# Kernel tuning notes

Measured on AMD Instinct MI355X. Metric: run time of the kernel, lower is better.

The kernel has to match this reference:

```python
import jax, jax.numpy as jnp
import numpy as np

HIDDEN = 256
HEADS = 8
HEAD_DIM = HIDDEN // HEADS
SCALE = HEAD_DIM ** -0.5
N = 4096
NUM_GRAPHS = 16
LN_EPS = 1e-5


def setup_inputs() -> dict:
    key = jax.random.key(0)
    ks = jax.random.split(key, 8)
    x = jax.random.normal(ks[0], (N, HIDDEN), dtype=jnp.float32)
    batch = jnp.sort(jax.random.randint(ks[1], (N,), 0, NUM_GRAPHS, dtype=jnp.int64))
    # Xavier-uniform linear weights, stored as [in, out] (y = x @ W + b)
    lim = float(np.sqrt(6.0 / (HIDDEN + HIDDEN)))
    def W(k):
        return jax.random.uniform(k, (HIDDEN, HIDDEN), jnp.float32, -lim, lim)
    return {
        "x": x,
        "batch": batch,
        "Wq": W(ks[2]), "bq": jnp.zeros((HIDDEN,), jnp.float32),
        "Wk": W(ks[3]), "bk": jnp.zeros((HIDDEN,), jnp.float32),
        "Wv": W(ks[4]), "bv": jnp.zeros((HIDDEN,), jnp.float32),
        "Wo": W(ks[5]), "bo": jnp.zeros((HIDDEN,), jnp.float32),
        "gamma": jnp.ones((HIDDEN,), jnp.float32),
        "beta": jnp.zeros((HIDDEN,), jnp.float32),
    }


def _layer_norm(x, gamma, beta):
    mu = jnp.mean(x, axis=-1, keepdims=True)
    var = jnp.mean(jnp.square(x - mu), axis=-1, keepdims=True)
    return (x - mu) * jax.lax.rsqrt(var + LN_EPS) * gamma + beta


def reference(x, batch, Wq, bq, Wk, bk, Wv, bv, Wo, bo, gamma, beta):
    residual = x
    h = _layer_norm(x, gamma, beta)
    n = h.shape[0]
    q = (h @ Wq + bq).reshape(n, HEADS, HEAD_DIM)
    k = (h @ Wk + bk).reshape(n, HEADS, HEAD_DIM)
    v = (h @ Wv + bv).reshape(n, HEADS, HEAD_DIM)
    # dense scores masked to block-diagonal (same-graph) structure
    scores = jnp.einsum('ihd,jhd->ihj', q, k) * SCALE  # [N, H, N]
    same_graph = (batch[None, :] == batch[:, None])[:, None, :]  # [N, 1, N]
    scores = jnp.where(same_graph, scores, -jnp.inf)
    attn = jax.nn.softmax(scores, axis=-1)
    attn = jnp.nan_to_num(attn, nan=0.0)
    out = jnp.einsum('ihj,jhd->ihd', attn, v).reshape(n, HIDDEN)
    out = out @ Wo + bo
    return residual + out
```

## Files before the change

### kernel.cpp

```cpp
#include <hip/hip_runtime.h>

#define NNODES 4096
#define HID 256
#define NG 16
#define NH 8
#define HD 32
#define LN_EPS 1e-5f
#define QSCALE (0.17677669529663687f * 1.4426950408889634f)
#define HLS 264

typedef unsigned short u16;
typedef unsigned int u32;
typedef __bf16 bf16x8 __attribute__((ext_vector_type(8)));
typedef float f32x4 __attribute__((ext_vector_type(4)));

__device__ __forceinline__ u16 f2bf(float f){
  union { float f; u32 i; } c; c.f = f;
  u32 x = c.i;
  return (u16)((x + 0x7fffu + ((x >> 16) & 1u)) >> 16);
}

__global__ __launch_bounds__(256) void lnqkv_kernel(
    const float* __restrict__ x, const float* __restrict__ gamma,
    const float* __restrict__ beta,
    const float* __restrict__ Wq, const float* __restrict__ Wk,
    const float* __restrict__ Wv,
    const float* __restrict__ bq, const float* __restrict__ bk,
    const float* __restrict__ bv,
    u16* __restrict__ qb, u16* __restrict__ kb, u16* __restrict__ vb){
  __shared__ u16 hl[64][HLS];
  int bid = blockIdx.x;
  int which = blockIdx.y;
  int wave = threadIdx.x >> 6, lane = threadIdx.x & 63;
  int m0 = (bid >> 2) * 64;
  int nb = (bid & 3) * 64 + wave * 16;
  const float* W    = (which == 0) ? Wq : (which == 1) ? Wk : Wv;
  const float* bias = (which == 0) ? bq : (which == 1) ? bk : bv;
  u16* out          = (which == 0) ? qb : (which == 1) ? kb : vb;

  int rsub = lane >> 4;
  int c16  = lane & 15;
  float4 g0 = *(const float4*)(gamma + c16 * 16 + 0);
  float4 g1 = *(const float4*)(gamma + c16 * 16 + 4);
  float4 g2 = *(const float4*)(gamma + c16 * 16 + 8);
  float4 g3 = *(const float4*)(gamma + c16 * 16 + 12);
  float4 t0 = *(const float4*)(beta + c16 * 16 + 0);
  float4 t1 = *(const float4*)(beta + c16 * 16 + 4);
  float4 t2 = *(const float4*)(beta + c16 * 16 + 8);
  float4 t3 = *(const float4*)(beta + c16 * 16 + 12);
  float ga[16] = {g0.x,g0.y,g0.z,g0.w, g1.x,g1.y,g1.z,g1.w,
                  g2.x,g2.y,g2.z,g2.w, g3.x,g3.y,g3.z,g3.w};
  float bt[16] = {t0.x,t0.y,t0.z,t0.w, t1.x,t1.y,t1.z,t1.w,
                  t2.x,t2.y,t2.z,t2.w, t3.x,t3.y,t3.z,t3.w};
  #pragma unroll
  for (int b = 0; b < 4; b++){
    int rloc = wave * 16 + b * 4 + rsub;
    const float* xr = x + (size_t)(m0 + rloc) * HID + c16 * 16;
    float4 v0 = *(const float4*)(xr + 0);
    float4 v1 = *(const float4*)(xr + 4);
    float4 v2 = *(const float4*)(xr + 8);
    float4 v3 = *(const float4*)(xr + 12);
    float e[16] = {v0.x,v0.y,v0.z,v0.w, v1.x,v1.y,v1.z,v1.w,
                   v2.x,v2.y,v2.z,v2.w, v3.x,v3.y,v3.z,v3.w};
    float s = 0.f;
    #pragma unroll
    for (int i = 0; i < 16; i++) s += e[i];
    s += __shfl_xor(s, 1); s += __shfl_xor(s, 2);
    s += __shfl_xor(s, 4); s += __shfl_xor(s, 8);
    float mu = s * (1.0f / HID);
    float vv = 0.f;
    #pragma unroll
    for (int i = 0; i < 16; i++){ e[i] -= mu; vv += e[i] * e[i]; }
    vv += __shfl_xor(vv, 1); vv += __shfl_xor(vv, 2);
    vv += __shfl_xor(vv, 4); vv += __shfl_xor(vv, 8);
    float rs = rsqrtf(vv * (1.0f / HID) + LN_EPS);
    u32 pk[8];
    #pragma unroll
    for (int i = 0; i < 8; i++){
      float o0 = e[2*i]     * rs * ga[2*i]     + bt[2*i];
      float o1 = e[2*i + 1] * rs * ga[2*i + 1] + bt[2*i + 1];
      pk[i] = (u32)f2bf(o0) | ((u32)f2bf(o1) << 16);
    }
    *(uint4*)&hl[rloc][c16 * 16]     = make_uint4(pk[0], pk[1], pk[2], pk[3]);
    *(uint4*)&hl[rloc][c16 * 16 + 8] = make_uint4(pk[4], pk[5], pk[6], pk[7]);
  }
  __syncthreads();

  int lr = lane & 15, lq = lane >> 4;
  f32x4 acc[4] = {};
  const float* wbase = W + nb + lr;
  #pragma unroll
  for (int k0 = 0; k0 < HID; k0 += 32){
    union { bf16x8 v; u16 e[8]; } bf;
    const float* wp = wbase + (size_t)(k0 + lq * 8) * HID;
    #pragma unroll
    for (int j = 0; j < 8; j++) bf.e[j] = f2bf(wp[(size_t)j * HID]);
    #pragma unroll
    for (int t = 0; t < 4; t++){
      bf16x8 a = *(const bf16x8*)&hl[t * 16 + lr][k0 + lq * 8];
      acc[t] = __builtin_amdgcn_mfma_f32_16x16x32_bf16(a, bf.v, acc[t], 0, 0, 0);
    }
  }
  int col = nb + lr;
  float bb = bias[col];
  #pragma unroll
  for (int t = 0; t < 4; t++){
    #pragma unroll
    for (int r = 0; r < 4; r++){
      int row = m0 + 16 * t + lq * 4 + r;
      out[(size_t)row * HID + col] = f2bf(acc[t][r] + bb);
    }
  }
}

__global__ __launch_bounds__(512, 4) void attn_kernel(const u16* __restrict__ q,
    const u16* __restrict__ k, const u16* __restrict__ v,
    const int* __restrict__ batch, int bstride, u16* __restrict__ out){
  __shared__ float mg[4][10][64];
  __shared__ int s_se[2];
  int gh = blockIdx.y;
  int g = gh >> 3, hd = gh & 7;
  int wave = threadIdx.x >> 6, lane = threadIdx.x & 63;
  if (wave < 2){
    int target = g + wave;
    int p = batch[(size_t)(lane * 64) * bstride];
    int c = __popcll(__ballot(p < target));
    int lo = 0;
    if (c > 0){
      int base = (c - 1) * 64 + 1;
      int idx = base + lane;
      int val = (idx < NNODES) ? batch[(size_t)idx * bstride] : 0x7fffffff;
      lo = base + __popcll(__ballot(val < target));
    }
    if (lane == 0) s_se[wave] = lo;
  }
  __syncthreads();
  int start = s_se[0], end = s_se[1];
  int len = end - start;
  if (len <= 0) return;
  int ntj = (len + 15) >> 4;
  int lq = lane >> 4, lr = lane & 15;
  int tl = wave & 3;
  int jh = wave >> 2;
  int nouter = (ntj + 15) >> 4;
  for (int it = 0; it < nouter; it++){
    int tq = it * 16 + blockIdx.x * 4 + tl;
    bool active = tq < ntj;
    int q0 = tq << 4;
    float m = -3.0e38f, l = 0.f;
    f32x4 o0 = {0.f,0.f,0.f,0.f}, o1 = {0.f,0.f,0.f,0.f};
    if (active){
      bf16x8 qf = *(const bf16x8*)&q[(size_t)(start + q0 + lr) * HID + hd * HD + lq * 8];
      int half = (ntj + 1) >> 1;
      int jt0 = jh ? half : 0;
      int jt1 = jh ? ntj : half;
      for (int jt = jt0; jt < jt1; jt++){
        int j0 = jt << 4;
        int krow = start + j0 + lr;
        if (krow > NNODES - 1) krow = NNODES - 1;
        bf16x8 kf = *(const bf16x8*)&k[(size_t)krow * HID + hd * HD + lq * 8];
        u16 va[4], vc[4];
        #pragma unroll
        for (int i = 0; i < 4; i++){
          int vrow = start + j0 + lq * 4 + i;
          if (vrow > NNODES - 1) vrow = NNODES - 1;
          const u16* vp = &v[(size_t)vrow * HID + hd * HD + lr];
          va[i] = vp[0];
          vc[i] = vp[16];
        }
        f32x4 st = __builtin_amdgcn_mfma_f32_16x16x32_bf16(kf, qf,
                     (f32x4){0.f,0.f,0.f,0.f}, 0, 0, 0);
        int jb = j0 + lq * 4;
        float s0 = (jb + 0 < len) ? st[0] * QSCALE : -3.0e38f;
        float s1 = (jb + 1 < len) ? st[1] * QSCALE : -3.0e38f;
        float s2 = (jb + 2 < len) ? st[2] * QSCALE : -3.0e38f;
        float s3 = (jb + 3 < len) ? st[3] * QSCALE : -3.0e38f;
        float tm = fmaxf(fmaxf(s0, s1), fmaxf(s2, s3));
        tm = fmaxf(tm, __shfl_xor(tm, 16));
        tm = fmaxf(tm, __shfl_xor(tm, 32));
        float mn = fmaxf(m, tm);
        float alpha = exp2f(m - mn);
        float p0 = exp2f(s0 - mn), p1 = exp2f(s1 - mn);
        float p2 = exp2f(s2 - mn), p3 = exp2f(s3 - mn);
        float ps = (p0 + p1) + (p2 + p3);
        ps += __shfl_xor(ps, 16);
        ps += __shfl_xor(ps, 32);
        l = l * alpha + ps;
        m = mn;
        union { bf16x8 v8; u32 w[4]; } pf, vf0, vf1;
        pf.w[0] = (u32)f2bf(p0) | ((u32)f2bf(p1) << 16);
        pf.w[1] = (u32)f2bf(p2) | ((u32)f2bf(p3) << 16);
        pf.w[2] = 0; pf.w[3] = 0;
        vf0.w[0] = (u32)va[0] | ((u32)va[1] << 16);
        vf0.w[1] = (u32)va[2] | ((u32)va[3] << 16);
        vf0.w[2] = 0; vf0.w[3] = 0;
        vf1.w[0] = (u32)vc[0] | ((u32)vc[1] << 16);
        vf1.w[1] = (u32)vc[2] | ((u32)vc[3] << 16);
        vf1.w[2] = 0; vf1.w[3] = 0;
        o0 = o0 * alpha;
        o1 = o1 * alpha;
        o0 = __builtin_amdgcn_mfma_f32_16x16x32_bf16(vf0.v8, pf.v8, o0, 0, 0, 0);
        o1 = __builtin_amdgcn_mfma_f32_16x16x32_bf16(vf1.v8, pf.v8, o1, 0, 0, 0);
      }
    }
    if (jh == 1){
      mg[tl][0][lane] = o0[0]; mg[tl][1][lane] = o0[1];
      mg[tl][2][lane] = o0[2]; mg[tl][3][lane] = o0[3];
      mg[tl][4][lane] = o1[0]; mg[tl][5][lane] = o1[1];
      mg[tl][6][lane] = o1[2]; mg[tl][7][lane] = o1[3];
      mg[tl][8][lane] = m;     mg[tl][9][lane] = l;
    }
    __syncthreads();
    if (jh == 0 && active && q0 + lr < len){
      float m2 = mg[tl][8][lane], l2 = mg[tl][9][lane];
      float mn = fmaxf(m, m2);
      float a  = exp2f(m - mn);
      float a2 = exp2f(m2 - mn);
      float lt = l * a + l2 * a2;
      float rl = 1.0f / lt;
      float r0 = (o0[0]*a + mg[tl][0][lane]*a2) * rl;
      float r1 = (o0[1]*a + mg[tl][1][lane]*a2) * rl;
      float r2 = (o0[2]*a + mg[tl][2][lane]*a2) * rl;
      float r3 = (o0[3]*a + mg[tl][3][lane]*a2) * rl;
      float r4 = (o1[0]*a + mg[tl][4][lane]*a2) * rl;
      float r5 = (o1[1]*a + mg[tl][5][lane]*a2) * rl;
      float r6 = (o1[2]*a + mg[tl][6][lane]*a2) * rl;
      float r7 = (o1[3]*a + mg[tl][7][lane]*a2) * rl;
      u16* orow = out + (size_t)(start + q0 + lr) * HID + hd * HD;
      int dbase = lq * 4;
      *(u32*)&orow[dbase]          = (u32)f2bf(r0) | ((u32)f2bf(r1) << 16);
      *(u32*)&orow[dbase + 2]      = (u32)f2bf(r2) | ((u32)f2bf(r3) << 16);
      *(u32*)&orow[16 + dbase]     = (u32)f2bf(r4) | ((u32)f2bf(r5) << 16);
      *(u32*)&orow[16 + dbase + 2] = (u32)f2bf(r6) | ((u32)f2bf(r7) << 16);
    }
    __syncthreads();
  }
}

__global__ __launch_bounds__(256) void proj_kernel(const u16* __restrict__ ao,
    const float* __restrict__ Wo, const float* __restrict__ bo,
    const float* __restrict__ x, float* __restrict__ out){
  int gw = blockIdx.x * 4 + (threadIdx.x >> 6);
  int lane = threadIdx.x & 63;
  int lr = lane & 15, lq = lane >> 4;
  int m0 = (gw >> 4) * 64;
  int n0 = (gw & 15) * 16;
  f32x4 acc[4] = {};
  const u16* arow = ao + (size_t)(m0 + lr) * HID + lq * 8;
  const float* wbase = Wo + n0 + lr;
  #pragma unroll
  for (int k0 = 0; k0 < HID; k0 += 32){
    union { bf16x8 v; u16 e[8]; } bf;
    const float* wp = wbase + (size_t)(k0 + lq * 8) * HID;
    #pragma unroll
    for (int j = 0; j < 8; j++) bf.e[j] = f2bf(wp[(size_t)j * HID]);
    #pragma unroll
    for (int t = 0; t < 4; t++){
      bf16x8 a = *(const bf16x8*)(arow + (size_t)t * 16 * HID + k0);
      acc[t] = __builtin_amdgcn_mfma_f32_16x16x32_bf16(a, bf.v, acc[t], 0, 0, 0);
    }
  }
  int col = n0 + lr;
  float bb = bo[col];
  #pragma unroll
  for (int t = 0; t < 4; t++){
    #pragma unroll
    for (int r = 0; r < 4; r++){
      size_t row = (size_t)(m0 + 16 * t + lq * 4 + r) * HID + col;
      out[row] = acc[t][r] + bb + x[row];
    }
  }
}

__global__ void sentinel_kernel(u32* __restrict__ out, int nwords){
  int i = blockIdx.x * 256 + threadIdx.x;
  if (i < nwords) out[i] = 0x46404640u;
}

extern "C" void kernel_launch(void* const* d_in, const int* in_sizes, int n_in,
                              void* d_out, int out_size, void* d_ws, size_t ws_size,
                              hipStream_t stream){
  const float* x   = (const float*)d_in[0];
  const int* batch = (const int*)d_in[1];
  const float* Wq = (const float*)d_in[2],  *bq = (const float*)d_in[3];
  const float* Wk = (const float*)d_in[4],  *bk = (const float*)d_in[5];
  const float* Wv = (const float*)d_in[6],  *bv = (const float*)d_in[7];
  const float* Wo = (const float*)d_in[8],  *bo = (const float*)d_in[9];
  const float* gamma = (const float*)d_in[10], *beta = (const float*)d_in[11];

  const size_t BUF  = (size_t)NNODES * HID * 2;
  const size_t NEED = 1024 + 4 * BUF;

  if (ws_size < NEED){
    int nwords = out_size / 2;
    sentinel_kernel<<<(nwords + 255) / 256, 256, 0, stream>>>((u32*)d_out, nwords);
    return;
  }

  int bstride = (in_sizes[1] >= NNODES * 8) ? 2 : 1;

  char* w = (char*)d_ws;
  u16* qb = (u16*)(w + 1024);
  u16* kb = qb + (size_t)NNODES * HID;
  u16* vb = kb + (size_t)NNODES * HID;
  u16* ao = vb + (size_t)NNODES * HID;

  lnqkv_kernel<<<dim3(256, 3), 256, 0, stream>>>(x, gamma, beta, Wq, Wk, Wv,
                                                 bq, bk, bv, qb, kb, vb);
  attn_kernel<<<dim3(4, NG * NH), 512, 0, stream>>>(qb, kb, vb, batch, bstride, ao);
  proj_kernel<<<256, 256, 0, stream>>>(ao, Wo, bo, x, (float*)d_out);
}
```

Measured before the change: 115.7 us.

## Fuse attention with output projection per 16-row query tile

Attention and output projection now run in one kernel. Each block takes 16 query rows, computes all 8 heads with two waves per head that split the key range, keeps the attention output in LDS, then does the Wo GEMM with a pre-transposed bf16 Wo built by extra blocks in the QKV kernel. This drops the attention-output round trip through global memory and one launch. In exchange each block scans the full key range of every graph its rows span and masks scores by per-key batch loads, which adds redundant K/V reads across blocks and extra per-key loads in the inner loop.

```diff
diff --git a/kernel.cpp b/kernel.cpp
--- a/kernel.cpp
+++ b/kernel.cpp
@@ -8,6 +8,7 @@
 #define LN_EPS 1e-5f
 #define QSCALE (0.17677669529663687f * 1.4426950408889634f)
 #define HLS 264
+#define AOS 264
 
 typedef unsigned short u16;
 typedef unsigned int u32;
@@ -24,13 +25,28 @@
     const float* __restrict__ x, const float* __restrict__ gamma,
     const float* __restrict__ beta,
     const float* __restrict__ Wq, const float* __restrict__ Wk,
-    const float* __restrict__ Wv,
+    const float* __restrict__ Wv, const float* __restrict__ Wo,
     const float* __restrict__ bq, const float* __restrict__ bk,
     const float* __restrict__ bv,
-    u16* __restrict__ qb, u16* __restrict__ kb, u16* __restrict__ vb){
+    u16* __restrict__ qb, u16* __restrict__ kb, u16* __restrict__ vb,
+    u16* __restrict__ WoT){
   __shared__ u16 hl[64][HLS];
   int bid = blockIdx.x;
   int which = blockIdx.y;
+  if (which == 3){
+    if (bid >= 64) return;
+    u16 (*tl)[33] = (u16(*)[33])hl;
+    int bx = (bid & 7) * 32, by = (bid >> 3) * 32;
+    int tx = threadIdx.x & 31, ty = threadIdx.x >> 5;
+    #pragma unroll
+    for (int r = 0; r < 32; r += 8)
+      tl[ty + r][tx] = f2bf(Wo[(size_t)(by + ty + r) * HID + bx + tx]);
+    __syncthreads();
+    #pragma unroll
+    for (int r = 0; r < 32; r += 8)
+      WoT[(size_t)(bx + ty + r) * HID + by + tx] = tl[tx][ty + r];
+    return;
+  }
   int wave = threadIdx.x >> 6, lane = threadIdx.x & 63;
   int m0 = (bid >> 2) * 64;
   int nb = (bid & 3) * 64 + wave * 16;
@@ -113,16 +129,21 @@
   }
 }
 
-__global__ __launch_bounds__(512, 4) void attn_kernel(const u16* __restrict__ q,
-    const u16* __restrict__ k, const u16* __restrict__ v,
-    const int* __restrict__ batch, int bstride, u16* __restrict__ out){
-  __shared__ float mg[4][10][64];
+__global__ __launch_bounds__(1024, 4) void attnproj_kernel(
+    const u16* __restrict__ q, const u16* __restrict__ k,
+    const u16* __restrict__ v, const u16* __restrict__ WoT,
+    const float* __restrict__ bo, const float* __restrict__ x,
+    const int* __restrict__ batch, int bstride, float* __restrict__ out){
+  __shared__ u16 ao[16][AOS];
+  __shared__ float mg[8][10][64];
   __shared__ int s_se[2];
-  int gh = blockIdx.y;
-  int g = gh >> 3, hd = gh & 7;
-  int wave = threadIdx.x >> 6, lane = threadIdx.x & 63;
+  int m0 = blockIdx.x * 16;
+  int tid = threadIdx.x;
+  int wave = tid >> 6, lane = tid & 63;
+  int g_lo = batch[(size_t)m0 * bstride];
+  int g_hi = batch[(size_t)(m0 + 15) * bstride];
   if (wave < 2){
-    int target = g + wave;
+    int target = wave ? (g_hi + 1) : g_lo;
     int p = batch[(size_t)(lane * 64) * bstride];
     int c = __popcll(__ballot(p < target));
     int lo = 0;
@@ -135,139 +156,124 @@
     if (lane == 0) s_se[wave] = lo;
   }
   __syncthreads();
-  int start = s_se[0], end = s_se[1];
-  int len = end - start;
-  if (len <= 0) return;
-  int ntj = (len + 15) >> 4;
+  int jstart = s_se[0], jend = s_se[1];
+  int ntj = (jend - jstart + 15) >> 4;
   int lq = lane >> 4, lr = lane & 15;
-  int tl = wave & 3;
-  int jh = wave >> 2;
-  int nouter = (ntj + 15) >> 4;
-  for (int it = 0; it < nouter; it++){
-    int tq = it * 16 + blockIdx.x * 4 + tl;
-    bool active = tq < ntj;
-    int q0 = tq << 4;
-    float m = -3.0e38f, l = 0.f;
-    f32x4 o0 = {0.f,0.f,0.f,0.f}, o1 = {0.f,0.f,0.f,0.f};
-    if (active){
-      bf16x8 qf = *(const bf16x8*)&q[(size_t)(start + q0 + lr) * HID + hd * HD + lq * 8];
-      int half = (ntj + 1) >> 1;
-      int jt0 = jh ? half : 0;
-      int jt1 = jh ? ntj : half;
-      for (int jt = jt0; jt < jt1; jt++){
-        int j0 = jt << 4;
-        int krow = start + j0 + lr;
-        if (krow > NNODES - 1) krow = NNODES - 1;
-        bf16x8 kf = *(const bf16x8*)&k[(size_t)krow * HID + hd * HD + lq * 8];
-        u16 va[4], vc[4];
-        #pragma unroll
-        for (int i = 0; i < 4; i++){
-          int vrow = start + j0 + lq * 4 + i;
-          if (vrow > NNODES - 1) vrow = NNODES - 1;
-          const u16* vp = &v[(size_t)vrow * HID + hd * HD + lr];
-          va[i] = vp[0];
-          vc[i] = vp[16];
-        }
-        f32x4 st = __builtin_amdgcn_mfma_f32_16x16x32_bf16(kf, qf,
-                     (f32x4){0.f,0.f,0.f,0.f}, 0, 0, 0);
-        int jb = j0 + lq * 4;
-        float s0 = (jb + 0 < len) ? st[0] * QSCALE : -3.0e38f;
-        float s1 = (jb + 1 < len) ? st[1] * QSCALE : -3.0e38f;
-        float s2 = (jb + 2 < len) ? st[2] * QSCALE : -3.0e38f;
-        float s3 = (jb + 3 < len) ? st[3] * QSCALE : -3.0e38f;
-        float tm = fmaxf(fmaxf(s0, s1), fmaxf(s2, s3));
-        tm = fmaxf(tm, __shfl_xor(tm, 16));
-        tm = fmaxf(tm, __shfl_xor(tm, 32));
-        float mn = fmaxf(m, tm);
-        float alpha = exp2f(m - mn);
-        float p0 = exp2f(s0 - mn), p1 = exp2f(s1 - mn);
-        float p2 = exp2f(s2 - mn), p3 = exp2f(s3 - mn);
-        float ps = (p0 + p1) + (p2 + p3);
-        ps += __shfl_xor(ps, 16);
-        ps += __shfl_xor(ps, 32);
-        l = l * alpha + ps;
-        m = mn;
-        union { bf16x8 v8; u32 w[4]; } pf, vf0, vf1;
-        pf.w[0] = (u32)f2bf(p0) | ((u32)f2bf(p1) << 16);
-        pf.w[1] = (u32)f2bf(p2) | ((u32)f2bf(p3) << 16);
-        pf.w[2] = 0; pf.w[3] = 0;
-        vf0.w[0] = (u32)va[0] | ((u32)va[1] << 16);
-        vf0.w[1] = (u32)va[2] | ((u32)va[3] << 16);
-        vf0.w[2] = 0; vf0.w[3] = 0;
-        vf1.w[0] = (u32)vc[0] | ((u32)vc[1] << 16);
-        vf1.w[1] = (u32)vc[2] | ((u32)vc[3] << 16);
-        vf1.w[2] = 0; vf1.w[3] = 0;
-        o0 = o0 * alpha;
-        o1 = o1 * alpha;
-        o0 = __builtin_amdgcn_mfma_f32_16x16x32_bf16(vf0.v8, pf.v8, o0, 0, 0, 0);
-        o1 = __builtin_amdgcn_mfma_f32_16x16x32_bf16(vf1.v8, pf.v8, o1, 0, 0, 0);
+  int hd = wave & 7;
+  int jh = wave >> 3;
+
+  int qrow = m0 + lr;
+  bf16x8 qf = *(const bf16x8*)&q[(size_t)qrow * HID + hd * HD + lq * 8];
+  int gq = batch[(size_t)qrow * bstride];
+  float m = -3.0e38f, l = 0.f;
+  f32x4 o0 = {0.f,0.f,0.f,0.f}, o1 = {0.f,0.f,0.f,0.f};
+  {
+    int half = (ntj + 1) >> 1;
+    int jt0 = jh ? half : 0;
+    int jt1 = jh ? ntj : half;
+    for (int jt = jt0; jt < jt1; jt++){
+      int j0 = jstart + (jt << 4);
+      int krow = j0 + lr; if (krow > NNODES - 1) krow = NNODES - 1;
+      bf16x8 kf = *(const bf16x8*)&k[(size_t)krow * HID + hd * HD + lq * 8];
+      u16 va[4], vc[4];
+      #pragma unroll
+      for (int i = 0; i < 4; i++){
+        int vrow = j0 + lq * 4 + i;
+        if (vrow > NNODES - 1) vrow = NNODES - 1;
+        const u16* vp = &v[(size_t)vrow * HID + hd * HD + lr];
+        va[i] = vp[0];
+        vc[i] = vp[16];
       }
-    }
-    if (jh == 1){
-      mg[tl][0][lane] = o0[0]; mg[tl][1][lane] = o0[1];
-      mg[tl][2][lane] = o0[2]; mg[tl][3][lane] = o0[3];
-      mg[tl][4][lane] = o1[0]; mg[tl][5][lane] = o1[1];
-      mg[tl][6][lane] = o1[2]; mg[tl][7][lane] = o1[3];
-      mg[tl][8][lane] = m;     mg[tl][9][lane] = l;
-    }
-    __syncthreads();
-    if (jh == 0 && active && q0 + lr < len){
-      float m2 = mg[tl][8][lane], l2 = mg[tl][9][lane];
-      float mn = fmaxf(m, m2);
-      float a  = exp2f(m - mn);
-      float a2 = exp2f(m2 - mn);
-      float lt = l * a + l2 * a2;
-      float rl = 1.0f / lt;
-      float r0 = (o0[0]*a + mg[tl][0][lane]*a2) * rl;
-      float r1 = (o0[1]*a + mg[tl][1][lane]*a2) * rl;
-      float r2 = (o0[2]*a + mg[tl][2][lane]*a2) * rl;
-      float r3 = (o0[3]*a + mg[tl][3][lane]*a2) * rl;
-      float r4 = (o1[0]*a + mg[tl][4][lane]*a2) * rl;
-      float r5 = (o1[1]*a + mg[tl][5][lane]*a2) * rl;
-      float r6 = (o1[2]*a + mg[tl][6][lane]*a2) * rl;
-      float r7 = (o1[3]*a + mg[tl][7][lane]*a2) * rl;
-      u16* orow = out + (size_t)(start + q0 + lr) * HID + hd * HD;
-      int dbase = lq * 4;
-      *(u32*)&orow[dbase]          = (u32)f2bf(r0) | ((u32)f2bf(r1) << 16);
-      *(u32*)&orow[dbase + 2]      = (u32)f2bf(r2) | ((u32)f2bf(r3) << 16);
-      *(u32*)&orow[16 + dbase]     = (u32)f2bf(r4) | ((u32)f2bf(r5) << 16);
-      *(u32*)&orow[16 + dbase + 2] = (u32)f2bf(r6) | ((u32)f2bf(r7) << 16);
-    }
-    __syncthreads();
-  }
-}
-
-__global__ __launch_bounds__(256) void proj_kernel(const u16* __restrict__ ao,
-    const float* __restrict__ Wo, const float* __restrict__ bo,
-    const float* __restrict__ x, float* __restrict__ out){
-  int gw = blockIdx.x * 4 + (threadIdx.x >> 6);
-  int lane = threadIdx.x & 63;
-  int lr = lane & 15, lq = lane >> 4;
-  int m0 = (gw >> 4) * 64;
-  int n0 = (gw & 15) * 16;
-  f32x4 acc[4] = {};
-  const u16* arow = ao + (size_t)(m0 + lr) * HID + lq * 8;
-  const float* wbase = Wo + n0 + lr;
-  #pragma unroll
-  for (int k0 = 0; k0 < HID; k0 += 32){
-    union { bf16x8 v; u16 e[8]; } bf;
-    const float* wp = wbase + (size_t)(k0 + lq * 8) * HID;
-    #pragma unroll
-    for (int j = 0; j < 8; j++) bf.e[j] = f2bf(wp[(size_t)j * HID]);
-    #pragma unroll
-    for (int t = 0; t < 4; t++){
-      bf16x8 a = *(const bf16x8*)(arow + (size_t)t * 16 * HID + k0);
-      acc[t] = __builtin_amdgcn_mfma_f32_16x16x32_bf16(a, bf.v, acc[t], 0, 0, 0);
-    }
-  }
-  int col = n0 + lr;
-  float bb = bo[col];
-  #pragma unroll
-  for (int t = 0; t < 4; t++){
+      f32x4 st = __builtin_amdgcn_mfma_f32_16x16x32_bf16(kf, qf,
+                   (f32x4){0.f,0.f,0.f,0.f}, 0, 0, 0);
+      int jb = j0 + lq * 4;
+      int i0 = jb + 0 > 4095 ? 4095 : jb + 0;
+      int i1 = jb + 1 > 4095 ? 4095 : jb + 1;
+      int i2 = jb + 2 > 4095 ? 4095 : jb + 2;
+      int i3 = jb + 3 > 4095 ? 4095 : jb + 3;
+      int gj0 = batch[(size_t)i0 * bstride];
+      int gj1 = batch[(size_t)i1 * bstride];
+      int gj2 = batch[(size_t)i2 * bstride];
+      int gj3 = batch[(size_t)i3 * bstride];
+      float s0 = (jb + 0 < jend && gj0 == gq) ? st[0] * QSCALE : -3.0e38f;
+      float s1 = (jb + 1 < jend && gj1 == gq) ? st[1] * QSCALE : -3.0e38f;
+      float s2 = (jb + 2 < jend && gj2 == gq) ? st[2] * QSCALE : -3.0e38f;
+      float s3 = (jb + 3 < jend && gj3 == gq) ? st[3] * QSCALE : -3.0e38f;
+      float tm = fmaxf(fmaxf(s0, s1), fmaxf(s2, s3));
+      tm = fmaxf(tm, __shfl_xor(tm, 16));
+      tm = fmaxf(tm, __shfl_xor(tm, 32));
+      float mn = fmaxf(m, tm);
+      float alpha = exp2f(m - mn);
+      float p0 = exp2f(s0 - mn), p1 = exp2f(s1 - mn);
+      float p2 = exp2f(s2 - mn), p3 = exp2f(s3 - mn);
+      float ps = (p0 + p1) + (p2 + p3);
+      ps += __shfl_xor(ps, 16);
+      ps += __shfl_xor(ps, 32);
+      l = l * alpha + ps;
+      m = mn;
+      union { bf16x8 v8; u32 w[4]; } pf, vf0, vf1;
+      pf.w[0] = (u32)f2bf(p0) | ((u32)f2bf(p1) << 16);
+      pf.w[1] = (u32)f2bf(p2) | ((u32)f2bf(p3) << 16);
+      pf.w[2] = 0; pf.w[3] = 0;
+      vf0.w[0] = (u32)va[0] | ((u32)va[1] << 16);
+      vf0.w[1] = (u32)va[2] | ((u32)va[3] << 16);
+      vf0.w[2] = 0; vf0.w[3] = 0;
+      vf1.w[0] = (u32)vc[0] | ((u32)vc[1] << 16);
+      vf1.w[1] = (u32)vc[2] | ((u32)vc[3] << 16);
+      vf1.w[2] = 0; vf1.w[3] = 0;
+      o0 = o0 * alpha;
+      o1 = o1 * alpha;
+      o0 = __builtin_amdgcn_mfma_f32_16x16x32_bf16(vf0.v8, pf.v8, o0, 0, 0, 0);
+      o1 = __builtin_amdgcn_mfma_f32_16x16x32_bf16(vf1.v8, pf.v8, o1, 0, 0, 0);
+    }
+  }
+  if (jh == 1){
+    mg[hd][0][lane] = o0[0]; mg[hd][1][lane] = o0[1];
+    mg[hd][2][lane] = o0[2]; mg[hd][3][lane] = o0[3];
+    mg[hd][4][lane] = o1[0]; mg[hd][5][lane] = o1[1];
+    mg[hd][6][lane] = o1[2]; mg[hd][7][lane] = o1[3];
+    mg[hd][8][lane] = m;     mg[hd][9][lane] = l;
+  }
+  __syncthreads();
+  if (jh == 0){
+    float m2 = mg[hd][8][lane], l2 = mg[hd][9][lane];
+    float mn = fmaxf(m, m2);
+    float a  = exp2f(m - mn);
+    float a2 = exp2f(m2 - mn);
+    float lt = l * a + l2 * a2;
+    float rl = 1.0f / lt;
+    float r0 = (o0[0]*a + mg[hd][0][lane]*a2) * rl;
+    float r1 = (o0[1]*a + mg[hd][1][lane]*a2) * rl;
+    float r2 = (o0[2]*a + mg[hd][2][lane]*a2) * rl;
+    float r3 = (o0[3]*a + mg[hd][3][lane]*a2) * rl;
+    float r4 = (o1[0]*a + mg[hd][4][lane]*a2) * rl;
+    float r5 = (o1[1]*a + mg[hd][5][lane]*a2) * rl;
+    float r6 = (o1[2]*a + mg[hd][6][lane]*a2) * rl;
+    float r7 = (o1[3]*a + mg[hd][7][lane]*a2) * rl;
+    int dbase = hd * HD + lq * 4;
+    *(u32*)&ao[lr][dbase]          = (u32)f2bf(r0) | ((u32)f2bf(r1) << 16);
+    *(u32*)&ao[lr][dbase + 2]      = (u32)f2bf(r2) | ((u32)f2bf(r3) << 16);
+    *(u32*)&ao[lr][dbase + 16]     = (u32)f2bf(r4) | ((u32)f2bf(r5) << 16);
+    *(u32*)&ao[lr][dbase + 16 + 2] = (u32)f2bf(r6) | ((u32)f2bf(r7) << 16);
+  }
+  __syncthreads();
+
+  {
+    int n0 = wave * 16;
+    f32x4 acc = {};
+    const u16* brow = WoT + (size_t)(n0 + lr) * HID + lq * 8;
+    #pragma unroll
+    for (int k0 = 0; k0 < HID; k0 += 32){
+      bf16x8 a = *(const bf16x8*)&ao[lr][k0 + lq * 8];
+      bf16x8 b = *(const bf16x8*)(brow + k0);
+      acc = __builtin_amdgcn_mfma_f32_16x16x32_bf16(a, b, acc, 0, 0, 0);
+    }
+    int col = n0 + lr;
+    float bb = bo[col];
     #pragma unroll
     for (int r = 0; r < 4; r++){
-      size_t row = (size_t)(m0 + 16 * t + lq * 4 + r) * HID + col;
-      out[row] = acc[t][r] + bb + x[row];
+      size_t idx = (size_t)(m0 + lq * 4 + r) * HID + col;
+      out[idx] = acc[r] + bb + x[idx];
     }
   }
 }
@@ -289,7 +295,8 @@
   const float* gamma = (const float*)d_in[10], *beta = (const float*)d_in[11];
 
   const size_t BUF  = (size_t)NNODES * HID * 2;
-  const size_t NEED = 1024 + 4 * BUF;
+  const size_t WOT  = (size_t)HID * HID * 2;
+  const size_t NEED = 1024 + 3 * BUF + WOT;
 
   if (ws_size < NEED){
     int nwords = out_size / 2;
@@ -300,13 +307,13 @@
   int bstride = (in_sizes[1] >= NNODES * 8) ? 2 : 1;
 
   char* w = (char*)d_ws;
-  u16* qb = (u16*)(w + 1024);
-  u16* kb = qb + (size_t)NNODES * HID;
-  u16* vb = kb + (size_t)NNODES * HID;
-  u16* ao = vb + (size_t)NNODES * HID;
-
-  lnqkv_kernel<<<dim3(256, 3), 256, 0, stream>>>(x, gamma, beta, Wq, Wk, Wv,
-                                                 bq, bk, bv, qb, kb, vb);
-  attn_kernel<<<dim3(4, NG * NH), 512, 0, stream>>>(qb, kb, vb, batch, bstride, ao);
-  proj_kernel<<<256, 256, 0, stream>>>(ao, Wo, bo, x, (float*)d_out);
-}
+  u16* qb  = (u16*)(w + 1024);
+  u16* kb  = qb + (size_t)NNODES * HID;
+  u16* vb  = kb + (size_t)NNODES * HID;
+  u16* WoT = vb + (size_t)NNODES * HID;
+
+  lnqkv_kernel<<<dim3(256, 4), 256, 0, stream>>>(x, gamma, beta, Wq, Wk, Wv, Wo,
+                                                 bq, bk, bv, qb, kb, vb, WoT);
+  attnproj_kernel<<<256, 1024, 0, stream>>>(qb, kb, vb, WoT, bo, x, batch,
+                                            bstride, (float*)d_out);
+}
```

Result: no change. 114.8 us (-0.8%).
